# Kernel tuning notes

Measured on AMD Instinct MI355X. Metric: run time of the kernel, lower is better.

## Reference

```python
import jax, jax.numpy as jnp
import numpy as np

N = 50000      # nodes
E = 1000000    # edges
NF = 5         # node_features
EF = 2         # edge_features
RS = 128       # rnn_size
RES = 32       # rnn_edge_size
H = 4          # heads
C = 16         # out_features
FIN = RS + RES # GAT in_channels
NEG_SLOPE = 0.2


def lstm_step(x, h, c, Wih, Whh, bih, bhh):
    # Single-step LSTM (torch gate order: i, f, g, o)
    g = x @ Wih.T + h @ Whh.T + bih + bhh
    i, f, gg, o = jnp.split(g, 4, axis=-1)
    i = jax.nn.sigmoid(i); f = jax.nn.sigmoid(f)
    gg = jnp.tanh(gg); o = jax.nn.sigmoid(o)
    c2 = f * c + i * gg
    return o * jnp.tanh(c2), c2


def setup_inputs() -> dict:
    key = jax.random.key(0)
    ks = jax.random.split(key, 20)
    p = lambda k, shape: (jax.random.normal(k, shape) * 0.1).astype(jnp.float32)
    return dict(
        x=jax.random.normal(ks[0], (N, NF), jnp.float32),
        edge_index=jax.random.randint(ks[1], (2, E), 0, N),
        edge_attr=jax.random.normal(ks[2], (E, EF), jnp.float32),
        h_node_h=p(ks[3], (N, RS)), h_node_c=p(ks[4], (N, RS)),
        h_edge_h=p(ks[5], (E, RES)), h_edge_c=p(ks[6], (E, RES)),
        Wih_n=p(ks[7], (4 * RS, NF)), Whh_n=p(ks[8], (4 * RS, RS)),
        bih_n=p(ks[9], (4 * RS,)), bhh_n=p(ks[10], (4 * RS,)),
        Wih_e=p(ks[11], (4 * RES, EF)), Whh_e=p(ks[12], (4 * RES, RES)),
        bih_e=p(ks[13], (4 * RES,)), bhh_e=p(ks[14], (4 * RES,)),
        W_gat=p(ks[15], (FIN, H * C)),
        att_src=p(ks[16], (H, C)), att_dst=p(ks[17], (H, C)),
        bias_gat=p(ks[18], (C,)),
    )


def reference(x, edge_index, edge_attr, h_node_h, h_node_c, h_edge_h, h_edge_c,
              Wih_n, Whh_n, bih_n, bhh_n, Wih_e, Whh_e, bih_e, bhh_e,
              W_gat, att_src, att_dst, bias_gat):
    n = x.shape[0]
    # --- edge history encoder: per-edge LSTM step + scatter-mean to dst nodes ---
    he, ce = lstm_step(edge_attr, h_edge_h, h_edge_c, Wih_e, Whh_e, bih_e, bhh_e)
    dst0 = edge_index[1]
    esum = jax.ops.segment_sum(he, dst0, num_segments=n)
    deg = jax.ops.segment_sum(jnp.ones((he.shape[0], 1), he.dtype), dst0, num_segments=n)
    edge_enc = esum / jnp.maximum(deg, 1.0)            # [N, RES]
    # --- node history encoder: per-node LSTM step ---
    hn, cn = lstm_step(x, h_node_h, h_node_c, Wih_n, Whh_n, bih_n, bhh_n)
    feat = jnp.concatenate([hn, edge_enc], axis=-1)    # [N, FIN]
    # --- GATConv (PyG v1 style, add_self_loops=True, concat=False) ---
    xl = (feat @ W_gat).reshape(n, H, C)               # [N, H, C]
    a_src = jnp.einsum('nhc,hc->nh', xl, att_src)
    a_dst = jnp.einsum('nhc,hc->nh', xl, att_dst)
    loops = jnp.arange(n)
    src = jnp.concatenate([edge_index[0], loops])
    dst = jnp.concatenate([edge_index[1], loops])
    alpha = jax.nn.leaky_relu(a_src[src] + a_dst[dst], NEG_SLOPE)  # [E+N, H]
    m = jax.ops.segment_max(alpha, dst, num_segments=n)
    ea = jnp.exp(alpha - m[dst])
    s = jax.ops.segment_sum(ea, dst, num_segments=n)
    w = ea / s[dst]                                     # segment softmax over dst
    out = jax.ops.segment_sum(xl[src] * w[:, :, None], dst, num_segments=n)  # [N,H,C]
    out = out.mean(axis=1) + bias_gat                   # concat=False -> head mean
    return (out, hn, cn, he, ce)
```

## Files before the change

### kernel.cpp

```cpp
#include <hip/hip_runtime.h>

#define CAP 64

typedef __attribute__((ext_vector_type(8))) short bf16x8;
typedef __attribute__((ext_vector_type(4))) float f32x4;

__device__ __forceinline__ float sigf(float x) {
    return __builtin_amdgcn_rcpf(1.0f + __expf(-x));
}
__device__ __forceinline__ float tanhfast(float x) {
    return 2.0f * __builtin_amdgcn_rcpf(1.0f + __expf(-2.0f * x)) - 1.0f;
}
__device__ __forceinline__ short bfr(float f) {
    unsigned u = __float_as_uint(f);
    unsigned r = (u + 0x7FFFu + ((u >> 16) & 1u)) >> 16;
    return (short)r;
}
__device__ __forceinline__ float bf2f(unsigned short u) {
    return __uint_as_float(((unsigned)u) << 16);
}
__device__ __forceinline__ bf16x8 cvt8(const float* p) {
    const float4* q = (const float4*)p;
    float4 u = q[0], v = q[1];
    bf16x8 r;
    r[0]=bfr(u.x); r[1]=bfr(u.y); r[2]=bfr(u.z); r[3]=bfr(u.w);
    r[4]=bfr(v.x); r[5]=bfr(v.y); r[6]=bfr(v.z); r[7]=bfr(v.w);
    return r;
}

__global__ void convert_kernel(
    const float* __restrict__ Whh_n, const float* __restrict__ Wih_n,
    const float* __restrict__ bih_n, const float* __restrict__ bhh_n,
    const float* __restrict__ Whh_e, const float* __restrict__ Wih_e,
    const float* __restrict__ bih_e, const float* __restrict__ bhh_e,
    const float* __restrict__ Wgat,
    unsigned short* __restrict__ WnF, unsigned short* __restrict__ WeF,
    unsigned short* __restrict__ WgF, int* __restrict__ cnt, int N)
{
    int i = blockIdx.x * 256 + threadIdx.x;
    if (i < N) cnt[i] = 0;
    if (i < 512 * 160) {
        int j = i & 7, unit = i >> 3;
        int lane = unit & 63, tk = unit >> 6;
        int tp = tk / 5, k4 = tk - tp * 5;
        int r = (tp & 3) * 128 + (tp >> 2) * 16 + (lane & 15);
        int k = k4 * 32 + (lane >> 4) * 8 + j;
        float v = (k < 128) ? Whh_n[r * 128 + k]
                : (k < 133) ? Wih_n[r * 5 + (k - 128)]
                : (k == 133) ? (bih_n[r] + bhh_n[r]) : 0.f;
        WnF[i] = (unsigned short)bfr(v);
    }
    if (i < 128 * 64) {
        int j = i & 7, unit = i >> 3;
        int lane = unit & 63, ts = unit >> 6;
        int t = ts >> 1, s = ts & 1;
        int r = t * 16 + (lane & 15);
        int k = s * 32 + (lane >> 4) * 8 + j;
        float v = (k < 32) ? Whh_e[r * 32 + k]
                : (k < 34) ? Wih_e[r * 2 + (k - 32)]
                : (k == 34) ? (bih_e[r] + bhh_e[r]) : 0.f;
        WeF[i] = (unsigned short)bfr(v);
    }
    if (i < 64 * 160) {
        int j = i & 7, unit = i >> 3;
        int lane = unit & 63, tk = unit >> 6;
        int t = tk / 5, k4 = tk - t * 5;
        int r = t * 16 + (lane & 15);
        int k = k4 * 32 + (lane >> 4) * 8 + j;
        WgF[i] = (unsigned short)bfr(Wgat[k * 64 + r]);
    }
}

__global__ void csr_fill_kernel(const int* __restrict__ src, const int* __restrict__ dst,
                                int* __restrict__ cnt, int2* __restrict__ eidp, int E)
{
    int e = blockIdx.x * blockDim.x + threadIdx.x;
    if (e >= E) return;
    int d = dst[e];
    int s = src[e];
    int k = atomicAdd(cnt + d, 1);
    if (k < CAP) eidp[(size_t)d * CAP + k] = make_int2(e, s);
}

__global__ __launch_bounds__(256, 3) void edge_lstm_mfma(
    const float* __restrict__ eattr, const float* __restrict__ h_in, const float* __restrict__ c_in,
    const unsigned short* __restrict__ WeF,
    float* __restrict__ he_out, float* __restrict__ ce_out, int E)
{
    __shared__ float Gall[4][16 * 132];
    __shared__ unsigned short Hall[4][16 * 40];
    const int lane = threadIdx.x & 63, wave = threadIdx.x >> 6;
    const int lr = lane & 15, lg = lane >> 4;
    const int T = E >> 4;
    const int nwaves = gridDim.x * 4;
    const int wid = blockIdx.x * 4 + wave;
    if (wid >= T) return;
    float* G = Gall[wave];
    unsigned short* H = Hall[wave];

    const bf16x8* Wv = (const bf16x8*)WeF;
    bf16x8 wa0[8], wa1[8];
    #pragma unroll
    for (int t = 0; t < 8; ++t) {
        wa0[t] = Wv[(t * 2 + 0) * 64 + lane];
        wa1[t] = Wv[(t * 2 + 1) * 64 + lane];
    }

    f32x4 phA, phB, pcA, pcB; float pea0 = 0.f, pea1 = 0.f;
    {
        const size_t dwb = (size_t)wid * 512;
        phA = *(const f32x4*)(h_in + dwb + lane * 4);
        phB = *(const f32x4*)(h_in + dwb + 256 + lane * 4);
        pcA = *(const f32x4*)(c_in + dwb + lane * 4);
        pcB = *(const f32x4*)(c_in + dwb + 256 + lane * 4);
        if (lg == 0) {
            pea0 = eattr[(size_t)(wid * 16 + lr) * 2];
            pea1 = eattr[(size_t)(wid * 16 + lr) * 2 + 1];
        }
    }

    for (int t = wid; t < T; t += nwaves) {
        const f32x4 hA = phA, hB = phB, cA = pcA, cB = pcB;
        const float ea0 = pea0, ea1 = pea1;
        const size_t dwbase = (size_t)t * 512;
        const int tn = t + nwaves;
        if (tn < T) {
            const size_t dwb = (size_t)tn * 512;
            phA = *(const f32x4*)(h_in + dwb + lane * 4);
            phB = *(const f32x4*)(h_in + dwb + 256 + lane * 4);
            pcA = *(const f32x4*)(c_in + dwb + lane * 4);
            pcB = *(const f32x4*)(c_in + dwb + 256 + lane * 4);
            if (lg == 0) {
                pea0 = eattr[(size_t)(tn * 16 + lr) * 2];
                pea1 = eattr[(size_t)(tn * 16 + lr) * 2 + 1];
            }
        }

        {
            const int e = lane >> 3, c4 = (lane & 7) * 4;
            ushort4 pa, pb;
            pa.x = (unsigned short)bfr(hA[0]); pa.y = (unsigned short)bfr(hA[1]);
            pa.z = (unsigned short)bfr(hA[2]); pa.w = (unsigned short)bfr(hA[3]);
            pb.x = (unsigned short)bfr(hB[0]); pb.y = (unsigned short)bfr(hB[1]);
            pb.z = (unsigned short)bfr(hB[2]); pb.w = (unsigned short)bfr(hB[3]);
            *(ushort4*)(H + e * 40 + c4)       = pa;
            *(ushort4*)(H + (8 + e) * 40 + c4) = pb;
        }
        bf16x8 b0 = *(const bf16x8*)(H + lr * 40 + lg * 8);
        bf16x8 b1 = {0,0,0,0,0,0,0,0};
        if (lg == 0) {
            b1[0] = bfr(ea0); b1[1] = bfr(ea1); b1[2] = (short)0x3F80;
        }

        f32x4 acc[8];
        #pragma unroll
        for (int tt = 0; tt < 8; ++tt) {
            f32x4 v = {0, 0, 0, 0};
            v = __builtin_amdgcn_mfma_f32_16x16x32_bf16(wa0[tt], b0, v, 0, 0, 0);
            v = __builtin_amdgcn_mfma_f32_16x16x32_bf16(wa1[tt], b1, v, 0, 0, 0);
            acc[tt] = v;
        }

        #pragma unroll
        for (int u = 0; u < 8; ++u) {
            const int col = (u >> 1) * 32 + (u & 1) * 16 + lg * 4;
            *(f32x4*)(G + lr * 132 + col) = acc[u];
        }

        const int e = lane >> 3, jq = (lane & 7) * 4;
        #pragma unroll
        for (int part = 0; part < 2; ++part) {
            const float* gr = G + (part * 8 + e) * 132;
            const f32x4 gi = *(const f32x4*)(gr + jq);
            const f32x4 gf = *(const f32x4*)(gr + 32 + jq);
            const f32x4 gg = *(const f32x4*)(gr + 64 + jq);
            const f32x4 go = *(const f32x4*)(gr + 96 + jq);
            const f32x4 cold = part ? cB : cA;
            f32x4 cres, hres;
            #pragma unroll
            for (int q = 0; q < 4; ++q) {
                float c2 = sigf(gf[q]) * cold[q] + sigf(gi[q]) * tanhfast(gg[q]);
                cres[q] = c2;
                hres[q] = sigf(go[q]) * tanhfast(c2);
            }
            __builtin_nontemporal_store(cres, (f32x4*)(ce_out + dwbase + part * 256 + lane * 4));
            *(f32x4*)(he_out + dwbase + part * 256 + lane * 4) = hres;
        }
    }
}

__global__ __launch_bounds__(256) void node_lstm_mfma(
    const float* __restrict__ x, const float* __restrict__ h_in, const float* __restrict__ c_in,
    const unsigned short* __restrict__ WnF,
    float* __restrict__ hn_out, float* __restrict__ cn_out, int N)
{
    const int lane = threadIdx.x & 63, wave = threadIdx.x >> 6;
    const int nbase = blockIdx.x * 64 + wave * 16;
    if (nbase >= N) return;
    const int lr = lane & 15, lg = lane >> 4;
    const int node = nbase + lr;
    bf16x8 b[5];
    const float* hp = h_in + (size_t)node * 128 + lg * 8;
    b[0] = cvt8(hp); b[1] = cvt8(hp + 32); b[2] = cvt8(hp + 64); b[3] = cvt8(hp + 96);
    bf16x8 bx = {0,0,0,0,0,0,0,0};
    if (lg == 0) {
        const float* xp = x + (size_t)node * 5;
        bx[0]=bfr(xp[0]); bx[1]=bfr(xp[1]); bx[2]=bfr(xp[2]); bx[3]=bfr(xp[3]); bx[4]=bfr(xp[4]);
        bx[5] = (short)0x3F80;
    }
    b[4] = bx;
    const bf16x8* Wv = (const bf16x8*)WnF;
    #pragma unroll
    for (int u = 0; u < 8; ++u) {
        f32x4 acc[4];
        #pragma unroll
        for (int g = 0; g < 4; ++g) {
            const bf16x8* ap = Wv + (u * 4 + g) * 320 + lane;
            f32x4 v = {0, 0, 0, 0};
            #pragma unroll
            for (int k4 = 0; k4 < 5; ++k4)
                v = __builtin_amdgcn_mfma_f32_16x16x32_bf16(ap[k4 * 64], b[k4], v, 0, 0, 0);
            acc[g] = v;
        }
        const int jb = u * 16 + lg * 4;
        f32x4 cold = *(const f32x4*)(c_in + (size_t)node * 128 + jb);
        f32x4 cres, hres;
        #pragma unroll
        for (int q = 0; q < 4; ++q) {
            float c2 = sigf(acc[1][q]) * cold[q] + sigf(acc[0][q]) * tanhfast(acc[2][q]);
            cres[q] = c2;
            hres[q] = sigf(acc[3][q]) * tanhfast(c2);
        }
        __builtin_nontemporal_store(cres, (f32x4*)(cn_out + (size_t)node * 128 + jb));
        *(f32x4*)(hn_out + (size_t)node * 128 + jb) = hres;
    }
}

__global__ __launch_bounds__(256) void enc_gatxl_kernel(
    const int* __restrict__ cnt, const int2* __restrict__ eidp, const float* __restrict__ he,
    const float* __restrict__ hn, const unsigned short* __restrict__ WgF,
    const float* __restrict__ attS, const float* __restrict__ attD,
    unsigned short* __restrict__ xlb, float* __restrict__ asrc, float* __restrict__ adst, int N)
{
    __shared__ float encs[64 * 36];
    const int lane = threadIdx.x & 63, wave = threadIdx.x >> 6;
    const int nbase = blockIdx.x * 64 + wave * 16;
    if (nbase >= N) return;
    const int half = lane >> 5, hl = lane & 31;
    const int g4 = hl >> 3, l8 = hl & 7;
    for (int t = 0; t < 16; t += 2) {
        const int node = nbase + t + half;
        const int c = cnt[node];
        const int m = min(c, CAP);
        const int2* el = eidp + (size_t)node * CAP;
        f32x4 acc = {0, 0, 0, 0};
        for (int i = g4; i < m; i += 4)
            acc += *(const f32x4*)(he + (size_t)el[i].x * 32 + l8 * 4);
        #pragma unroll
        for (int off = 8; off <= 16; off <<= 1) {
            acc[0] += __shfl_xor(acc[0], off);
            acc[1] += __shfl_xor(acc[1], off);
            acc[2] += __shfl_xor(acc[2], off);
            acc[3] += __shfl_xor(acc[3], off);
        }
        if (g4 == 0) {
            float inv = 1.0f / fmaxf((float)c, 1.0f);
            f32x4 r; r[0]=acc[0]*inv; r[1]=acc[1]*inv; r[2]=acc[2]*inv; r[3]=acc[3]*inv;
            *(f32x4*)(&encs[(wave * 16 + t + half) * 36 + l8 * 4]) = r;
        }
    }
    const int lr = lane & 15, lg = lane >> 4;
    const int node = nbase + lr;
    bf16x8 b[5];
    const float* hp = hn + (size_t)node * 128 + lg * 8;
    b[0] = cvt8(hp); b[1] = cvt8(hp + 32); b[2] = cvt8(hp + 64); b[3] = cvt8(hp + 96);
    b[4] = cvt8(&encs[(wave * 16 + lr) * 36 + lg * 8]);
    const bf16x8* Wv = (const bf16x8*)WgF;
    #pragma unroll
    for (int t = 0; t < 4; ++t) {
        const bf16x8* ap = Wv + t * 320 + lane;
        f32x4 v = {0, 0, 0, 0};
        #pragma unroll
        for (int k4 = 0; k4 < 5; ++k4)
            v = __builtin_amdgcn_mfma_f32_16x16x32_bf16(ap[k4 * 64], b[k4], v, 0, 0, 0);
        ushort4 pk;
        pk.x = (unsigned short)bfr(v[0]); pk.y = (unsigned short)bfr(v[1]);
        pk.z = (unsigned short)bfr(v[2]); pk.w = (unsigned short)bfr(v[3]);
        *(ushort4*)(xlb + (size_t)node * 64 + t * 16 + lg * 4) = pk;
        const f32x4 ws = *(const f32x4*)(attS + t * 16 + lg * 4);
        const f32x4 wd = *(const f32x4*)(attD + t * 16 + lg * 4);
        float p1 = v[0]*ws[0] + v[1]*ws[1] + v[2]*ws[2] + v[3]*ws[3];
        float p2 = v[0]*wd[0] + v[1]*wd[1] + v[2]*wd[2] + v[3]*wd[3];
        p1 += __shfl_xor(p1, 16); p2 += __shfl_xor(p2, 16);
        p1 += __shfl_xor(p1, 32); p2 += __shfl_xor(p2, 32);
        if (lg == 0) {
            asrc[(size_t)node * 4 + t] = p1;
            adst[(size_t)node * 4 + t] = p2;
        }
    }
}

__global__ __launch_bounds__(256) void gat_node_kernel(
    const int* __restrict__ cnt, const int2* __restrict__ eidp,
    const float* __restrict__ asrc, const float* __restrict__ adst,
    const unsigned short* __restrict__ xlb, const float* __restrict__ bias,
    float* __restrict__ out, int N)
{
    const int wid = (blockIdx.x * blockDim.x + threadIdx.x) >> 6;
    const int lane = threadIdx.x & 63;
    if (wid >= N) return;
    const int n = wid;
    const int m = min(cnt[n], CAP);
    const int h = lane >> 4, c16 = lane & 15;
    const int nslot = (m + 15) >> 4;
    const float ad = adst[n * 4 + h];
    float aself = asrc[n * 4 + h] + ad;
    aself = aself > 0.f ? aself : 0.2f * aself;
    const int2* el = eidp + (size_t)n * CAP;
    int   ss[4];
    float aa[4];
    float mx = aself;
    #pragma unroll
    for (int k = 0; k < 4; ++k) {
        if (k >= nslot) break;
        int i = k * 16 + c16;
        if (i < m) {
            int s = el[i].y;
            float a = asrc[s * 4 + h] + ad;
            a = a > 0.f ? a : 0.2f * a;
            ss[k] = s; aa[k] = a;
            mx = fmaxf(mx, a);
        } else { ss[k] = 0; aa[k] = -1e30f; }
    }
    #pragma unroll
    for (int off = 1; off < 16; off <<= 1) mx = fmaxf(mx, __shfl_xor(mx, off));
    float ea[4];
    float p = 0.f;
    #pragma unroll
    for (int k = 0; k < 4; ++k) {
        if (k >= nslot) break;
        ea[k] = __expf(aa[k] - mx);
        p += ea[k];
    }
    #pragma unroll
    for (int off = 1; off < 16; off <<= 1) p += __shfl_xor(p, off);
    float eself = __expf(aself - mx);
    float sacc = eself + p;
    float oacc = eself * bf2f(xlb[(size_t)n * 64 + lane]);
    const int grp = lane & 48;
    #pragma unroll
    for (int k = 0; k < 4; ++k) {
        if (k >= nslot) break;
        const int lim = min(16, m - k * 16);
        #pragma unroll 4
        for (int cc = 0; cc < lim; ++cc) {
            int srcl = grp | cc;
            float w = __shfl(ea[k], srcl);
            int   s = __shfl(ss[k], srcl);
            oacc += w * bf2f(xlb[(size_t)s * 64 + lane]);
        }
    }
    float r = oacc / sacc;
    r += __shfl_xor(r, 16);
    r += __shfl_xor(r, 32);
    if (lane < 16) out[(size_t)n * 16 + lane] = 0.25f * r + bias[lane];
}

extern "C" void kernel_launch(void* const* d_in, const int* in_sizes, int n_in,
                              void* d_out, int out_size, void* d_ws, size_t ws_size,
                              hipStream_t stream)
{
    const float* x     = (const float*)d_in[0];
    const int*   ei    = (const int*)  d_in[1];
    const float* eattr = (const float*)d_in[2];
    const float* hn_h  = (const float*)d_in[3];
    const float* hn_c  = (const float*)d_in[4];
    const float* he_h  = (const float*)d_in[5];
    const float* he_c  = (const float*)d_in[6];
    const float* Wih_n = (const float*)d_in[7];
    const float* Whh_n = (const float*)d_in[8];
    const float* bih_n = (const float*)d_in[9];
    const float* bhh_n = (const float*)d_in[10];
    const float* Wih_e = (const float*)d_in[11];
    const float* Whh_e = (const float*)d_in[12];
    const float* bih_e = (const float*)d_in[13];
    const float* bhh_e = (const float*)d_in[14];
    const float* W_gat = (const float*)d_in[15];
    const float* attS  = (const float*)d_in[16];
    const float* attD  = (const float*)d_in[17];
    const float* biasG = (const float*)d_in[18];

    const int N = in_sizes[0] / 5;
    const int E = in_sizes[2] / 2;

    float* out = (float*)d_out;
    float* hn  = out + (size_t)N * 16;
    float* cn  = hn  + (size_t)N * 128;
    float* he  = cn  + (size_t)N * 128;
    float* ce  = he  + (size_t)E * 32;

    char* p = (char*)d_ws;
    size_t off = 0;
    auto take = [&](size_t bytes) -> void* {
        void* r = p + off;
        off = (off + bytes + 255) & ~(size_t)255;
        return r;
    };
    int*   cnt  = (int*)  take((size_t)N * 4);
    int2*  eidp = (int2*) take((size_t)N * CAP * 8);
    unsigned short* xlb = (unsigned short*)take((size_t)N * 64 * 2);
    float* asrc = (float*)take((size_t)N * 4 * 4);
    float* adst = (float*)take((size_t)N * 4 * 4);
    unsigned short* WnF = (unsigned short*)take(512 * 160 * 2);
    unsigned short* WeF = (unsigned short*)take(128 * 64 * 2);
    unsigned short* WgF = (unsigned short*)take(64 * 160 * 2);

    convert_kernel<<<(512 * 160 + 255) / 256, 256, 0, stream>>>(
        Whh_n, Wih_n, bih_n, bhh_n, Whh_e, Wih_e, bih_e, bhh_e, W_gat,
        WnF, WeF, WgF, cnt, N);
    csr_fill_kernel<<<(E + 255) / 256, 256, 0, stream>>>(ei, ei + E, cnt, eidp, E);
    edge_lstm_mfma<<<768, 256, 0, stream>>>(
        eattr, he_h, he_c, WeF, he, ce, E);
    node_lstm_mfma<<<(N + 63) / 64, 256, 0, stream>>>(
        x, hn_h, hn_c, WnF, hn, cn, N);
    enc_gatxl_kernel<<<(N + 63) / 64, 256, 0, stream>>>(
        cnt, eidp, he, hn, WgF, attS, attD, xlb, asrc, adst, N);
    gat_node_kernel<<<(N + 3) / 4, 256, 0, stream>>>(
        cnt, eidp, asrc, adst, xlb, biasG, out, N);
}
```

Measured before the change: 351.1 us.

## Fuse node LSTM into encoder/GAT projection kernel, passing hn via LDS

Merges the node LSTM kernel with the edge-mean encoder and GAT linear projection kernel. The new hidden state is written to global memory for output and also kept as bf16 in per-wave shared memory, where the projection MFMA reads it. This removes one launch and the global re-read of hn (25.6 MB). The hn store also becomes nontemporal. In exchange, LDS use per block grows by about 17 KB, which may lower occupancy, and the fused kernel carries more register pressure.

After: 374.5 us. +6.7%, slower.

```diff
diff --git a/kernel.cpp b/kernel.cpp
--- a/kernel.cpp
+++ b/kernel.cpp
@@ -189,70 +189,73 @@
     }
 }
 
-__global__ __launch_bounds__(256) void node_lstm_mfma(
+__global__ __launch_bounds__(256) void node_enc_gatxl_kernel(
     const float* __restrict__ x, const float* __restrict__ h_in, const float* __restrict__ c_in,
     const unsigned short* __restrict__ WnF,
-    float* __restrict__ hn_out, float* __restrict__ cn_out, int N)
-{
-    const int lane = threadIdx.x & 63, wave = threadIdx.x >> 6;
-    const int nbase = blockIdx.x * 64 + wave * 16;
-    if (nbase >= N) return;
-    const int lr = lane & 15, lg = lane >> 4;
-    const int node = nbase + lr;
-    bf16x8 b[5];
-    const float* hp = h_in + (size_t)node * 128 + lg * 8;
-    b[0] = cvt8(hp); b[1] = cvt8(hp + 32); b[2] = cvt8(hp + 64); b[3] = cvt8(hp + 96);
-    bf16x8 bx = {0,0,0,0,0,0,0,0};
-    if (lg == 0) {
-        const float* xp = x + (size_t)node * 5;
-        bx[0]=bfr(xp[0]); bx[1]=bfr(xp[1]); bx[2]=bfr(xp[2]); bx[3]=bfr(xp[3]); bx[4]=bfr(xp[4]);
-        bx[5] = (short)0x3F80;
-    }
-    b[4] = bx;
-    const bf16x8* Wv = (const bf16x8*)WnF;
-    #pragma unroll
-    for (int u = 0; u < 8; ++u) {
-        f32x4 acc[4];
-        #pragma unroll
-        for (int g = 0; g < 4; ++g) {
-            const bf16x8* ap = Wv + (u * 4 + g) * 320 + lane;
-            f32x4 v = {0, 0, 0, 0};
-            #pragma unroll
-            for (int k4 = 0; k4 < 5; ++k4)
-                v = __builtin_amdgcn_mfma_f32_16x16x32_bf16(ap[k4 * 64], b[k4], v, 0, 0, 0);
-            acc[g] = v;
-        }
-        const int jb = u * 16 + lg * 4;
-        f32x4 cold = *(const f32x4*)(c_in + (size_t)node * 128 + jb);
-        f32x4 cres, hres;
-        #pragma unroll
-        for (int q = 0; q < 4; ++q) {
-            float c2 = sigf(acc[1][q]) * cold[q] + sigf(acc[0][q]) * tanhfast(acc[2][q]);
-            cres[q] = c2;
-            hres[q] = sigf(acc[3][q]) * tanhfast(c2);
-        }
-        __builtin_nontemporal_store(cres, (f32x4*)(cn_out + (size_t)node * 128 + jb));
-        *(f32x4*)(hn_out + (size_t)node * 128 + jb) = hres;
-    }
-}
-
-__global__ __launch_bounds__(256) void enc_gatxl_kernel(
+    float* __restrict__ hn_out, float* __restrict__ cn_out,
     const int* __restrict__ cnt, const int2* __restrict__ eidp, const float* __restrict__ he,
-    const float* __restrict__ hn, const unsigned short* __restrict__ WgF,
+    const unsigned short* __restrict__ WgF,
     const float* __restrict__ attS, const float* __restrict__ attD,
     unsigned short* __restrict__ xlb, float* __restrict__ asrc, float* __restrict__ adst, int N)
 {
+    __shared__ unsigned short hball[4][16 * 136];
     __shared__ float encs[64 * 36];
     const int lane = threadIdx.x & 63, wave = threadIdx.x >> 6;
     const int nbase = blockIdx.x * 64 + wave * 16;
     if (nbase >= N) return;
+    unsigned short* H = hball[wave];
+    const int lr = lane & 15, lg = lane >> 4;
+    const int node = nbase + lr;
+
+    {
+        bf16x8 b[5];
+        const float* hp = h_in + (size_t)node * 128 + lg * 8;
+        b[0] = cvt8(hp); b[1] = cvt8(hp + 32); b[2] = cvt8(hp + 64); b[3] = cvt8(hp + 96);
+        bf16x8 bx = {0,0,0,0,0,0,0,0};
+        if (lg == 0) {
+            const float* xp = x + (size_t)node * 5;
+            bx[0]=bfr(xp[0]); bx[1]=bfr(xp[1]); bx[2]=bfr(xp[2]); bx[3]=bfr(xp[3]); bx[4]=bfr(xp[4]);
+            bx[5] = (short)0x3F80;
+        }
+        b[4] = bx;
+        const bf16x8* Wv = (const bf16x8*)WnF;
+        #pragma unroll
+        for (int u = 0; u < 8; ++u) {
+            f32x4 acc[4];
+            #pragma unroll
+            for (int g = 0; g < 4; ++g) {
+                const bf16x8* ap = Wv + (u * 4 + g) * 320 + lane;
+                f32x4 v = {0, 0, 0, 0};
+                #pragma unroll
+                for (int k4 = 0; k4 < 5; ++k4)
+                    v = __builtin_amdgcn_mfma_f32_16x16x32_bf16(ap[k4 * 64], b[k4], v, 0, 0, 0);
+                acc[g] = v;
+            }
+            const int jb = u * 16 + lg * 4;
+            f32x4 cold = *(const f32x4*)(c_in + (size_t)node * 128 + jb);
+            f32x4 cres, hres;
+            #pragma unroll
+            for (int q = 0; q < 4; ++q) {
+                float c2 = sigf(acc[1][q]) * cold[q] + sigf(acc[0][q]) * tanhfast(acc[2][q]);
+                cres[q] = c2;
+                hres[q] = sigf(acc[3][q]) * tanhfast(c2);
+            }
+            __builtin_nontemporal_store(cres, (f32x4*)(cn_out + (size_t)node * 128 + jb));
+            __builtin_nontemporal_store(hres, (f32x4*)(hn_out + (size_t)node * 128 + jb));
+            ushort4 hh;
+            hh.x = (unsigned short)bfr(hres[0]); hh.y = (unsigned short)bfr(hres[1]);
+            hh.z = (unsigned short)bfr(hres[2]); hh.w = (unsigned short)bfr(hres[3]);
+            *(ushort4*)(H + lr * 136 + jb) = hh;
+        }
+    }
+
     const int half = lane >> 5, hl = lane & 31;
     const int g4 = hl >> 3, l8 = hl & 7;
     for (int t = 0; t < 16; t += 2) {
-        const int node = nbase + t + half;
-        const int c = cnt[node];
+        const int nd = nbase + t + half;
+        const int c = cnt[nd];
         const int m = min(c, CAP);
-        const int2* el = eidp + (size_t)node * CAP;
+        const int2* el = eidp + (size_t)nd * CAP;
         f32x4 acc = {0, 0, 0, 0};
         for (int i = g4; i < m; i += 4)
             acc += *(const f32x4*)(he + (size_t)el[i].x * 32 + l8 * 4);
@@ -269,11 +272,12 @@
             *(f32x4*)(&encs[(wave * 16 + t + half) * 36 + l8 * 4]) = r;
         }
     }
-    const int lr = lane & 15, lg = lane >> 4;
-    const int node = nbase + lr;
+
     bf16x8 b[5];
-    const float* hp = hn + (size_t)node * 128 + lg * 8;
-    b[0] = cvt8(hp); b[1] = cvt8(hp + 32); b[2] = cvt8(hp + 64); b[3] = cvt8(hp + 96);
+    b[0] = *(const bf16x8*)(H + lr * 136 + lg * 8);
+    b[1] = *(const bf16x8*)(H + lr * 136 + 32 + lg * 8);
+    b[2] = *(const bf16x8*)(H + lr * 136 + 64 + lg * 8);
+    b[3] = *(const bf16x8*)(H + lr * 136 + 96 + lg * 8);
     b[4] = cvt8(&encs[(wave * 16 + lr) * 36 + lg * 8]);
     const bf16x8* Wv = (const bf16x8*)WgF;
     #pragma unroll
@@ -421,10 +425,9 @@
     csr_fill_kernel<<<(E + 255) / 256, 256, 0, stream>>>(ei, ei + E, cnt, eidp, E);
     edge_lstm_mfma<<<768, 256, 0, stream>>>(
         eattr, he_h, he_c, WeF, he, ce, E);
-    node_lstm_mfma<<<(N + 63) / 64, 256, 0, stream>>>(
-        x, hn_h, hn_c, WnF, hn, cn, N);
-    enc_gatxl_kernel<<<(N + 63) / 64, 256, 0, stream>>>(
-        cnt, eidp, he, hn, WgF, attS, attD, xlb, asrc, adst, N);
+    node_enc_gatxl_kernel<<<(N + 63) / 64, 256, 0, stream>>>(
+        x, hn_h, hn_c, WnF, hn, cn,
+        cnt, eidp, he, WgF, attS, attD, xlb, asrc, adst, N);
     gat_node_kernel<<<(N + 3) / 4, 256, 0, stream>>>(
         cnt, eidp, asrc, adst, xlb, biasG, out, N);
 }
```
